# Kernel tuning notes

Measured on AMD Instinct MI355X. Metric: run time of the kernel, lower is better.

Reference implementation:

```python
import jax, jax.numpy as jnp
import numpy as np

MIN_NORM = 1e-15
PROJ_EPS = 4e-3  # hgcn PoincareBall eps for float32
C = 1.0          # curvature (constant across both layers)


def _norm(x):
    return jnp.clip(jnp.linalg.norm(x, axis=-1, keepdims=True), MIN_NORM)


def _artanh(x):
    return jnp.arctanh(jnp.clip(x, -1.0 + 1e-7, 1.0 - 1e-7))


def proj(x, c):
    # clip points inside the Poincare ball of curvature c
    n = _norm(x)
    maxnorm = (1.0 - PROJ_EPS) / jnp.sqrt(c)
    return jnp.where(n > maxnorm, x / n * maxnorm, x)


def expmap0(u, c):
    sc = jnp.sqrt(c)
    n = _norm(u)
    return jnp.tanh(sc * n) * u / (sc * n)


def logmap0(p, c):
    sc = jnp.sqrt(c)
    n = _norm(p)
    return _artanh(sc * n) * p / (sc * n)


def mobius_add(x, y, c):
    x2 = jnp.sum(x * x, -1, keepdims=True)
    y2 = jnp.sum(y * y, -1, keepdims=True)
    xy = jnp.sum(x * y, -1, keepdims=True)
    num = (1.0 + 2.0 * c * xy + c * y2) * x + (1.0 - c * x2) * y
    den = 1.0 + 2.0 * c * xy + (c ** 2) * x2 * y2
    return num / jnp.clip(den, MIN_NORM)


def mobius_matvec(W, x, c):
    sc = jnp.sqrt(c)
    xn = _norm(x)
    mx = x @ W.T
    mxn = _norm(mx)
    res = jnp.tanh(mxn / xn * _artanh(sc * xn)) * mx / (mxn * sc)
    zero = jnp.all(mx == 0, axis=-1, keepdims=True)
    return jnp.where(zero, jnp.zeros((), x.dtype), res)


def hgc_layer(x, W, b, src, dst, ew, c_in, c_out, N):
    # HypLinear: mobius matvec + hyperbolic bias
    h = proj(mobius_matvec(W, x, c_in), c_in)
    hyp_b = proj(expmap0(b[None, :], c_in), c_in)  # proj_tan0 is identity
    h = proj(mobius_add(h, hyp_b, c_in), c_in)
    # HypAgg: tangent-space sparse aggregation
    xt = logmap0(h, c_in)                               # [N, d]
    msg = ew[:, None] * xt[src]                          # [E, d] gather
    agg = jax.ops.segment_sum(msg, dst, num_segments=N)  # spmm(adj, xt)
    h = proj(expmap0(agg, c_in), c_in)
    # HypAct: relu in tangent space, remap with c_out
    xt = jax.nn.relu(logmap0(h, c_in))
    return proj(expmap0(xt, c_out), c_out)


def setup_inputs() -> dict:
    key = jax.random.key(0)
    ks = jax.random.split(key, 8)
    N, F, H, D, E = 100000, 128, 128, 128, 1600000
    s = 1.0 / np.sqrt(F)
    x = jax.random.normal(ks[0], (N, F), jnp.float32) * 0.1
    W1 = jax.random.normal(ks[1], (H, F), jnp.float32) * s
    b1 = jax.random.normal(ks[2], (H,), jnp.float32) * 0.01
    W2 = jax.random.normal(ks[3], (D, H), jnp.float32) * s
    b2 = jax.random.normal(ks[4], (D,), jnp.float32) * 0.01
    edge_weight = jax.random.uniform(ks[5], (E,), jnp.float32) * (1.0 / 16.0)
    src = jax.random.randint(ks[6], (E,), 0, N)
    dst = jax.random.randint(ks[7], (E,), 0, N)
    return {"x": x, "W1": W1, "b1": b1, "W2": W2, "b2": b2,
            "edge_weight": edge_weight, "src": src, "dst": dst}


def reference(x, W1, b1, W2, b2, edge_weight, src, dst):
    N = x.shape[0]
    # HGCN.encode: map Euclidean features onto the manifold
    xh = proj(expmap0(x, C), C)  # proj_tan0 is identity for PoincareBall
    h = hgc_layer(xh, W1, b1, src, dst, edge_weight, C, C, N)
    h = hgc_layer(h, W2, b2, src, dst, edge_weight, C, C, N)
    return h
```

## Files before the change

### kernel.cpp

```cpp
#include <hip/hip_runtime.h>
#include <hip/hip_bf16.h>

#define MINN 1e-15f
#define MAXN (1.0f - 4e-3f)
#define ATMAX 3.1063031f

#define NBH 9
#define BNODES 512
#define BCAP 10240
#define BWIN (BCAP + 4 * BNODES)
#define PBE 8192

typedef short short8 __attribute__((ext_vector_type(8)));
typedef float f32x4 __attribute__((ext_vector_type(4)));

__device__ __forceinline__ float wsum(float v) {
    v += __shfl_xor(v, 32, 64);
    v += __shfl_xor(v, 16, 64);
    v += __shfl_xor(v, 8, 64);
    v += __shfl_xor(v, 4, 64);
    v += __shfl_xor(v, 2, 64);
    v += __shfl_xor(v, 1, 64);
    return v;
}

__device__ __forceinline__ void splitf(float f, short& hi, short& lo) {
    unsigned u = __float_as_uint(f);
    hi = (short)(u >> 16);
    float r = f - __uint_as_float(u & 0xffff0000u);
    lo = (short)(__float_as_uint(r) >> 16);
}

__device__ __forceinline__ unsigned packsplit_hi(short ha, short hb) {
    return (unsigned)(unsigned short)ha | ((unsigned)(unsigned short)hb << 16);
}

__device__ __forceinline__ unsigned pack_bf16(float a, float b) {
    unsigned ua = __float_as_uint(a);
    unsigned ub = __float_as_uint(b);
    ua = (ua + 0x7fffu + ((ua >> 16) & 1u)) >> 16;
    ub = (ub + 0x7fffu + ((ub >> 16) & 1u)) & 0xffff0000u;
    return ua | ub;
}

__device__ __forceinline__ float tanh_fast(float x) {
    float e = __expf(2.f * x);
    return (e - 1.f) * __builtin_amdgcn_rcpf(e + 1.f);
}
__device__ __forceinline__ float atanh_fast(float x) {
    return 0.5f * __logf((1.f + x) * __builtin_amdgcn_rcpf(1.f - x));
}

__global__ __launch_bounds__(256) void k_bucket(const int* __restrict__ src, const int* __restrict__ dst,
                                                const float* __restrict__ ew, int* __restrict__ gcur,
                                                int2* __restrict__ staging, int E, int NBUCK) {
    __shared__ int hist[512];
    const int tid = threadIdx.x;
    const int e0 = blockIdx.x * PBE;
    for (int i = tid; i < 512; i += 256) hist[i] = 0;
    __syncthreads();
    #pragma unroll 4
    for (int j = 0; j < PBE / 256; j++) {
        int e = e0 + j * 256 + tid;
        if (e < E) atomicAdd(&hist[dst[e] >> NBH], 1);
    }
    __syncthreads();
    for (int b = tid; b < NBUCK; b += 256) {
        int c = hist[b];
        hist[b] = c ? atomicAdd(&gcur[b], c) : 0;
    }
    __syncthreads();
    #pragma unroll 4
    for (int j = 0; j < PBE / 256; j++) {
        int e = e0 + j * 256 + tid;
        if (e < E) {
            int d = dst[e];
            int bkt = d >> NBH;
            int pos = atomicAdd(&hist[bkt], 1);
            if (pos < BCAP)
                staging[(size_t)bkt * BCAP + pos] =
                    make_int2((src[e] & 0x1FFFF) | ((d & (BNODES - 1)) << 17), __float_as_int(ew[e]));
        }
    }
}

__global__ __launch_bounds__(256) void k_cbuild(const int* __restrict__ gcur, const int2* __restrict__ staging,
                                                int2* __restrict__ csr, int2* __restrict__ rp2, int N) {
    __shared__ int cnt[BNODES];
    __shared__ int base[BNODES];
    __shared__ int sbuf[256];
    const int tid = threadIdx.x;
    const int b = blockIdx.x;
    const int bcnt = min(gcur[b], BCAP);
    const int wbase = b * BWIN;
    const int2* st = staging + (size_t)b * BCAP;

    for (int i = tid; i < BNODES; i += 256) cnt[i] = 0;
    __syncthreads();
    for (int i = tid; i < bcnt; i += 256) {
        int nl = (st[i].x >> 17) & (BNODES - 1);
        atomicAdd(&cnt[nl], 1);
    }
    __syncthreads();
    int p0 = (cnt[2 * tid] + 3) & ~3;
    int p1 = (cnt[2 * tid + 1] + 3) & ~3;
    int s = p0 + p1;
    sbuf[tid] = s;
    __syncthreads();
    for (int off = 1; off < 256; off <<= 1) {
        int add = (tid >= off) ? sbuf[tid - off] : 0;
        __syncthreads();
        sbuf[tid] += add;
        __syncthreads();
    }
    int excl = sbuf[tid] - s;
    base[2 * tid] = excl;
    base[2 * tid + 1] = excl + p0;
    __syncthreads();
    for (int i = tid; i < BNODES; i += 256) {
        int node = b * BNODES + i;
        int c = cnt[i];
        int pd = (c + 3) & ~3;
        int gb = wbase + base[i];
        if (node < N) rp2[node] = make_int2(gb, pd);
        for (int k = c; k < pd; k++) csr[gb + k] = make_int2(0, 0);
    }
    __syncthreads();
    for (int i = tid; i < BNODES; i += 256) cnt[i] = wbase + base[i];
    __syncthreads();
    for (int i = tid; i < bcnt; i += 256) {
        int2 p = st[i];
        int nl = (p.x >> 17) & (BNODES - 1);
        int pos = atomicAdd(&cnt[nl], 1);
        csr[pos] = make_int2(p.x & 0x1FFFF, p.y);
    }
}

__global__ __launch_bounds__(256) void k_wprep(const float* __restrict__ W1, const float* __restrict__ W2,
                                               unsigned* __restrict__ WH1, unsigned* __restrict__ WL1,
                                               unsigned* __restrict__ WH2, unsigned* __restrict__ WL2) {
    int i = (blockIdx.x & 31) * 256 + threadIdx.x;
    const float* W = (blockIdx.x < 32) ? W1 : W2;
    unsigned* WH = (blockIdx.x < 32) ? WH1 : WH2;
    unsigned* WL = (blockIdx.x < 32) ? WL1 : WL2;
    float a = W[2 * i], b = W[2 * i + 1];
    short ha, la, hb, lb;
    splitf(a, ha, la); splitf(b, hb, lb);
    WH[i] = packsplit_hi(ha, hb);
    WL[i] = packsplit_hi(la, lb);
}

__global__ __launch_bounds__(64) void k_bias(const float* __restrict__ B1, const float* __restrict__ B2,
                                             float2* __restrict__ HB) {
    const int lane = threadIdx.x;
    const float* B = (blockIdx.x == 0) ? B1 : B2;
    float2 bb = *(const float2*)(B + 2 * lane);
    float nb2 = wsum(bb.x * bb.x + bb.y * bb.y);
    float nb = fmaxf(sqrtf(nb2), MINN);
    float tbc = fminf(tanh_fast(nb), MAXN);
    float fb = tbc / nb;
    HB[blockIdx.x * 65 + lane] = make_float2(fb * bb.x, fb * bb.y);
    if (lane == 0) HB[blockIdx.x * 65 + 64] = make_float2(tbc * tbc, 0.f);
}

template <int ENCODE>
__global__ __launch_bounds__(256) void k_linear(
    const float* __restrict__ X,
    const unsigned* __restrict__ XH, const unsigned* __restrict__ XL,
    const unsigned* __restrict__ WH, const unsigned* __restrict__ WL,
    const float2* __restrict__ HB, const float2* __restrict__ NRM,
    unsigned* __restrict__ OUT, int N)
{
    __shared__ float pmn[4][16][4];
    __shared__ float pdm[4][16][4];

    const int lane = threadIdx.x & 63;
    const int wid = threadIdx.x >> 6;
    const int lr = lane & 15;
    const int lg = lane >> 4;
    const int tbase = blockIdx.x * 4;

    short8 Bh[2][4], Bl[2][4];
    #pragma unroll
    for (int ct = 0; ct < 2; ct++) {
        const int nrow = wid * 32 + 2 * lr + ct;
        #pragma unroll
        for (int kt = 0; kt < 4; kt++) {
            Bh[ct][kt] = *(const short8*)(WH + nrow * 64 + kt * 16 + lg * 4);
            Bl[ct][kt] = *(const short8*)(WL + nrow * 64 + kt * 16 + lg * 4);
        }
    }
    const float2 hbc = HB[wid * 16 + lr];
    const float y2 = HB[64].x;

    f32x4 acc[4][2];
    float xnr[4];

    #pragma unroll
    for (int t = 0; t < 4; t++) {
        const int row0 = (tbase + t) << 4;
        if (row0 >= N) break;
        const int arow = min(row0 + lr, N - 1);

        short8 Ah[4], Al[4];
        if (ENCODE) {
            float xn2 = 0.f;
            const float* xr = X + (size_t)arow * 128 + lg * 8;
            #pragma unroll
            for (int kt = 0; kt < 4; kt++) {
                float4 a0 = *(const float4*)(xr + kt * 32);
                float4 a1 = *(const float4*)(xr + kt * 32 + 4);
                float av[8] = {a0.x, a0.y, a0.z, a0.w, a1.x, a1.y, a1.z, a1.w};
                #pragma unroll
                for (int i = 0; i < 8; i++) {
                    xn2 = fmaf(av[i], av[i], xn2);
                    short h, l; splitf(av[i], h, l);
                    Ah[kt][i] = h; Al[kt][i] = l;
                }
            }
            xn2 += __shfl_xor(xn2, 16, 64);
            xn2 += __shfl_xor(xn2, 32, 64);
            xnr[t] = xn2;
        } else {
            #pragma unroll
            for (int kt = 0; kt < 4; kt++) {
                Ah[kt] = *(const short8*)(XH + (size_t)arow * 64 + kt * 16 + lg * 4);
                Al[kt] = *(const short8*)(XL + (size_t)arow * 64 + kt * 16 + lg * 4);
            }
        }

        f32x4 a0 = {0.f, 0.f, 0.f, 0.f}, a1 = {0.f, 0.f, 0.f, 0.f};
        #pragma unroll
        for (int kt = 0; kt < 4; kt++) {
            a0 = __builtin_amdgcn_mfma_f32_16x16x32_bf16(Ah[kt], Bh[0][kt], a0, 0, 0, 0);
            a1 = __builtin_amdgcn_mfma_f32_16x16x32_bf16(Ah[kt], Bh[1][kt], a1, 0, 0, 0);
            a0 = __builtin_amdgcn_mfma_f32_16x16x32_bf16(Al[kt], Bh[0][kt], a0, 0, 0, 0);
            a1 = __builtin_amdgcn_mfma_f32_16x16x32_bf16(Al[kt], Bh[1][kt], a1, 0, 0, 0);
            a0 = __builtin_amdgcn_mfma_f32_16x16x32_bf16(Ah[kt], Bl[0][kt], a0, 0, 0, 0);
            a1 = __builtin_amdgcn_mfma_f32_16x16x32_bf16(Ah[kt], Bl[1][kt], a1, 0, 0, 0);
        }
        acc[t][0] = a0; acc[t][1] = a1;

        float pm[4], pd[4];
        #pragma unroll
        for (int r = 0; r < 4; r++) {
            pm[r] = a0[r] * a0[r] + a1[r] * a1[r];
            pd[r] = a0[r] * hbc.x + a1[r] * hbc.y;
        }
        #pragma unroll
        for (int s = 1; s <= 8; s <<= 1) {
            #pragma unroll
            for (int r = 0; r < 4; r++) {
                pm[r] += __shfl_xor(pm[r], s, 64);
                pd[r] += __shfl_xor(pd[r], s, 64);
            }
        }
        if (lr == 0) {
            #pragma unroll
            for (int r = 0; r < 4; r++) {
                pmn[t][lg * 4 + r][wid] = pm[r];
                pdm[t][lg * 4 + r][wid] = pd[r];
            }
        }
    }
    __syncthreads();

    #pragma unroll
    for (int t = 0; t < 4; t++) {
        const int row0 = (tbase + t) << 4;
        if (row0 >= N) break;

        float4 qm = *(const float4*)pmn[t][lr];
        float4 qd = *(const float4*)pdm[t][lr];
        float mn2 = (qm.x + qm.y) + (qm.z + qm.w);
        float dmb = (qd.x + qd.y) + (qd.z + qd.w);
        const int crow = row0 + lr;
        float caf1 = 0.f, cbs = 0.f;
        if (crow < N) {
            float xn, axn;
            if (ENCODE) {
                float n0 = fmaxf(sqrtf(xnr[t]), MINN);
                xn = n0;
                axn = fminf(n0, ATMAX);
            } else {
                float2 nr = NRM[crow];
                xn = fmaxf(nr.x, MINN);
                axn = nr.y;
            }
            float mxn = fmaxf(sqrtf(mn2), MINN);
            float arg = (mxn / xn) * axn;
            float thc = fminf(tanh_fast(arg), MAXN);
            float f1 = thc / mxn;
            float x2 = thc * thc;
            float xy = f1 * dmb;
            float ca = 1.f + 2.f * xy + y2;
            float cb = 1.f - x2;
            float inv = 1.f / fmaxf(1.f + 2.f * xy + x2 * y2, MINN);
            float ng2 = inv * inv * (ca * ca * x2 + 2.f * ca * cb * xy + cb * cb * y2);
            float ng = fmaxf(sqrtf(ng2), MINN);
            float lf = atanh_fast(fminf(ng, MAXN)) / ng;
            float sle = lf * inv;
            caf1 = sle * ca * f1;
            cbs = sle * cb;
        }
        #pragma unroll
        for (int r = 0; r < 4; r++) {
            const int q = lg * 4 + r;
            float c1 = __shfl(caf1, q, 16);
            float c2 = __shfl(cbs, q, 16);
            const int row = row0 + q;
            if (row < N) {
                float o0 = c1 * acc[t][0][r] + c2 * hbc.x;
                float o1 = c1 * acc[t][1][r] + c2 * hbc.y;
                OUT[(size_t)row * 64 + wid * 16 + lr] = pack_bf16(o0, o1);
            }
        }
    }
}

__global__ __launch_bounds__(256) void k_aggact(const unsigned* __restrict__ XT, const int2* __restrict__ rp2,
                                                const int2* __restrict__ csr,
                                                float* __restrict__ OUTF,
                                                unsigned* __restrict__ OUTH, unsigned* __restrict__ OUTL,
                                                float2* __restrict__ NRM, int N, int last) {
    const int lane = threadIdx.x & 63;
    const int wid = threadIdx.x >> 6;
    int node = blockIdx.x * 4 + wid;
    if (node >= N) return;
    int2 rr = rp2[node];
    int b = __builtin_amdgcn_readfirstlane(rr.x);
    int cnt = __builtin_amdgcn_readfirstlane(rr.y);
    int e8 = b + (cnt & ~7);

    float ax[8], ay[8];
    #pragma unroll
    for (int j = 0; j < 8; j++) { ax[j] = 0.f; ay[j] = 0.f; }

    for (int i = b; i < e8; i += 8) {
        int2 c[8];
        #pragma unroll
        for (int j = 0; j < 8; j++) c[j] = csr[i + j];
        unsigned v[8];
        #pragma unroll
        for (int j = 0; j < 8; j++) v[j] = XT[(size_t)c[j].x * 64 + lane];
        #pragma unroll
        for (int j = 0; j < 8; j++) {
            float w = __int_as_float(c[j].y);
            ax[j] = fmaf(w, __uint_as_float(v[j] << 16), ax[j]);
            ay[j] = fmaf(w, __uint_as_float(v[j] & 0xffff0000u), ay[j]);
        }
    }
    if (cnt & 4) {
        int i = e8;
        int2 c[4];
        #pragma unroll
        for (int j = 0; j < 4; j++) c[j] = csr[i + j];
        unsigned v[4];
        #pragma unroll
        for (int j = 0; j < 4; j++) v[j] = XT[(size_t)c[j].x * 64 + lane];
        #pragma unroll
        for (int j = 0; j < 4; j++) {
            float w = __int_as_float(c[j].y);
            ax[j] = fmaf(w, __uint_as_float(v[j] << 16), ax[j]);
            ay[j] = fmaf(w, __uint_as_float(v[j] & 0xffff0000u), ay[j]);
        }
    }
    float a0 = ((ax[0] + ax[1]) + (ax[2] + ax[3])) + ((ax[4] + ax[5]) + (ax[6] + ax[7]));
    float a1 = ((ay[0] + ay[1]) + (ay[2] + ay[3])) + ((ay[4] + ay[5]) + (ay[6] + ay[7]));

    float r0 = fmaxf(a0, 0.f), r1 = fmaxf(a1, 0.f);
    float n2 = a0 * a0 + a1 * a1;
    float q2 = r0 * r0 + r1 * r1;
    #pragma unroll
    for (int s = 32; s; s >>= 1) {
        n2 += __shfl_xor(n2, s, 64);
        q2 += __shfl_xor(q2, s, 64);
    }
    float n = fmaxf(sqrtf(n2), MINN);
    float cp = fminf(n, ATMAX) / n;
    float nq = fmaxf(cp * sqrtf(q2), MINN);
    float tq = fminf(tanh_fast(nq), MAXN);
    float f2 = tq / nq;
    float sc = f2 * cp;
    float o0 = sc * r0, o1 = sc * r1;
    if (last) {
        *(float2*)(OUTF + (size_t)node * 128 + 2 * lane) = make_float2(o0, o1);
    } else {
        short h0, l0, h1, l1;
        splitf(o0, h0, l0); splitf(o1, h1, l1);
        OUTH[(size_t)node * 64 + lane] = packsplit_hi(h0, h1);
        OUTL[(size_t)node * 64 + lane] = packsplit_hi(l0, l1);
        if (lane == 0) NRM[node] = make_float2(tq, fminf(nq, ATMAX));
    }
}

extern "C" void kernel_launch(void* const* d_in, const int* in_sizes, int n_in,
                              void* d_out, int out_size, void* d_ws, size_t ws_size,
                              hipStream_t stream) {
    const float* x  = (const float*)d_in[0];
    const float* W1 = (const float*)d_in[1];
    const float* b1 = (const float*)d_in[2];
    const float* W2 = (const float*)d_in[3];
    const float* b2 = (const float*)d_in[4];
    const float* ew = (const float*)d_in[5];
    const int* src  = (const int*)d_in[6];
    const int* dst  = (const int*)d_in[7];
    const int N = in_sizes[0] / 128;
    const int E = in_sizes[5];
    float* out = (float*)d_out;

    const int NBUCK = (N + BNODES - 1) >> NBH;
    const int EB = (E + PBE - 1) / PBE;

    char* w = (char*)d_ws;
    unsigned* xt  = (unsigned*)w; w += (size_t)N * 64 * 4;
    unsigned* xh  = (unsigned*)w; w += (size_t)N * 64 * 4;
    unsigned* xl  = (unsigned*)w; w += (size_t)N * 64 * 4;
    int2*   csr   = (int2*)w;   w += (size_t)NBUCK * BWIN * 8;
    float2* nrm   = (float2*)w; w += (size_t)N * 8;
    int2*   rp2   = (int2*)w;   w += (size_t)N * 8;
    int2*   staging = (int2*)w; w += (size_t)NBUCK * BCAP * 8;
    unsigned* wh1 = (unsigned*)w; w += 8192 * 4;
    unsigned* wl1 = (unsigned*)w; w += 8192 * 4;
    unsigned* wh2 = (unsigned*)w; w += 8192 * 4;
    unsigned* wl2 = (unsigned*)w; w += 8192 * 4;
    float2* hbuf  = (float2*)w; w += 2 * 65 * 8;
    int*    gcur  = (int*)w;    w += (size_t)NBUCK * 4 + 256;

    hipMemsetAsync(gcur, 0, (size_t)NBUCK * 4, stream);
    k_bucket<<<EB, 256, 0, stream>>>(src, dst, ew, gcur, staging, E, NBUCK);
    k_cbuild<<<NBUCK, 256, 0, stream>>>(gcur, staging, csr, rp2, N);
    k_wprep<<<64, 256, 0, stream>>>(W1, W2, wh1, wl1, wh2, wl2);
    k_bias<<<2, 64, 0, stream>>>(b1, b2, hbuf);

    const int rowblocks = (N + 3) / 4;
    const int ntiles = (N + 15) / 16;
    const int nlb = (ntiles + 3) / 4;

    k_linear<1><<<nlb, 256, 0, stream>>>(x, nullptr, nullptr, wh1, wl1, hbuf, nullptr, xt, N);
    k_aggact<<<rowblocks, 256, 0, stream>>>(xt, rp2, csr, nullptr, xh, xl, nrm, N, 0);
    k_linear<0><<<nlb, 256, 0, stream>>>(nullptr, xh, xl, wh2, wl2, hbuf + 65, nrm, xt, N);
    k_aggact<<<rowblocks, 256, 0, stream>>>(xt, rp2, csr, out, nullptr, nullptr, nullptr, N, 1);
}
```

Before: 300.9 us.

## Store split-bf16 activations and weights in MFMA fragment order; add separate encode pass

Activations (hi/lo bf16 split) and weight matrices are now written in a fragment-major layout, so each lane's MFMA operand load becomes a contiguous 16-byte read at fragment base plus lane*4. Encoding of the input x moves out of the first linear kernel into a new k_encode kernel that splits values and records norms, so one k_linear serves both layers. The aim is coalesced operand loads in k_linear. The cost is an extra launch plus writing and rereading the split input, and aggact now does scattered fragment-index stores.

```diff
diff --git a/kernel.cpp b/kernel.cpp
--- a/kernel.cpp
+++ b/kernel.cpp
@@ -49,6 +49,10 @@
 }
 __device__ __forceinline__ float atanh_fast(float x) {
     return 0.5f * __logf((1.f + x) * __builtin_amdgcn_rcpf(1.f - x));
+}
+
+__device__ __forceinline__ size_t fragidx(int row, int c) {
+    return ((size_t)((row >> 4) * 4 + (c >> 4)) << 8) + ((((c >> 2) & 3) * 16 + (row & 15)) << 2) + (c & 3);
 }
 
 __global__ __launch_bounds__(256) void k_bucket(const int* __restrict__ src, const int* __restrict__ dst,
@@ -139,15 +143,21 @@
 __global__ __launch_bounds__(256) void k_wprep(const float* __restrict__ W1, const float* __restrict__ W2,
                                                unsigned* __restrict__ WH1, unsigned* __restrict__ WL1,
                                                unsigned* __restrict__ WH2, unsigned* __restrict__ WL2) {
-    int i = (blockIdx.x & 31) * 256 + threadIdx.x;
+    int f = (blockIdx.x & 31) * 256 + threadIdx.x;
     const float* W = (blockIdx.x < 32) ? W1 : W2;
     unsigned* WH = (blockIdx.x < 32) ? WH1 : WH2;
     unsigned* WL = (blockIdx.x < 32) ? WL1 : WL2;
-    float a = W[2 * i], b = W[2 * i + 1];
+    int frag = f >> 8, rem = f & 255;
+    int lane = rem >> 2, j = rem & 3;
+    int lr = lane & 15, lg = lane >> 4;
+    int wid = frag >> 3, ct = (frag >> 2) & 1, kt = frag & 3;
+    int n = wid * 32 + 2 * lr + ct;
+    int c = kt * 16 + lg * 4 + j;
+    float a = W[n * 128 + 2 * c], b = W[n * 128 + 2 * c + 1];
     short ha, la, hb, lb;
     splitf(a, ha, la); splitf(b, hb, lb);
-    WH[i] = packsplit_hi(ha, hb);
-    WL[i] = packsplit_hi(la, lb);
+    WH[f] = packsplit_hi(ha, hb);
+    WL[f] = packsplit_hi(la, lb);
 }
 
 __global__ __launch_bounds__(64) void k_bias(const float* __restrict__ B1, const float* __restrict__ B2,
@@ -163,11 +173,29 @@
     if (lane == 0) HB[blockIdx.x * 65 + 64] = make_float2(tbc * tbc, 0.f);
 }
 
-template <int ENCODE>
+__global__ __launch_bounds__(256) void k_encode(const float* __restrict__ X,
+                                                unsigned* __restrict__ XH, unsigned* __restrict__ XL,
+                                                float2* __restrict__ NRM, int N) {
+    const int lane = threadIdx.x & 63;
+    const int wid = threadIdx.x >> 6;
+    int row = blockIdx.x * 4 + wid;
+    if (row >= N) return;
+    float2 u = *(const float2*)(X + (size_t)row * 128 + 2 * lane);
+    float n2 = wsum(u.x * u.x + u.y * u.y);
+    short h0, l0, h1, l1;
+    splitf(u.x, h0, l0); splitf(u.y, h1, l1);
+    size_t idx = fragidx(row, lane);
+    XH[idx] = packsplit_hi(h0, h1);
+    XL[idx] = packsplit_hi(l0, l1);
+    if (lane == 0) {
+        float n0 = fmaxf(sqrtf(n2), MINN);
+        NRM[row] = make_float2(n0, fminf(n0, ATMAX));
+    }
+}
+
 __global__ __launch_bounds__(256) void k_linear(
-    const float* __restrict__ X,
-    const unsigned* __restrict__ XH, const unsigned* __restrict__ XL,
-    const unsigned* __restrict__ WH, const unsigned* __restrict__ WL,
+    const unsigned* __restrict__ XHf, const unsigned* __restrict__ XLf,
+    const unsigned* __restrict__ WHf, const unsigned* __restrict__ WLf,
     const float2* __restrict__ HB, const float2* __restrict__ NRM,
     unsigned* __restrict__ OUT, int N)
 {
@@ -183,50 +211,29 @@
     short8 Bh[2][4], Bl[2][4];
     #pragma unroll
     for (int ct = 0; ct < 2; ct++) {
-        const int nrow = wid * 32 + 2 * lr + ct;
         #pragma unroll
         for (int kt = 0; kt < 4; kt++) {
-            Bh[ct][kt] = *(const short8*)(WH + nrow * 64 + kt * 16 + lg * 4);
-            Bl[ct][kt] = *(const short8*)(WL + nrow * 64 + kt * 16 + lg * 4);
+            const int fb = ((wid * 2 + ct) * 4 + kt) << 8;
+            Bh[ct][kt] = *(const short8*)(WHf + fb + lane * 4);
+            Bl[ct][kt] = *(const short8*)(WLf + fb + lane * 4);
         }
     }
     const float2 hbc = HB[wid * 16 + lr];
     const float y2 = HB[64].x;
 
     f32x4 acc[4][2];
-    float xnr[4];
 
     #pragma unroll
     for (int t = 0; t < 4; t++) {
         const int row0 = (tbase + t) << 4;
         if (row0 >= N) break;
-        const int arow = min(row0 + lr, N - 1);
 
         short8 Ah[4], Al[4];
-        if (ENCODE) {
-            float xn2 = 0.f;
-            const float* xr = X + (size_t)arow * 128 + lg * 8;
-            #pragma unroll
-            for (int kt = 0; kt < 4; kt++) {
-                float4 a0 = *(const float4*)(xr + kt * 32);
-                float4 a1 = *(const float4*)(xr + kt * 32 + 4);
-                float av[8] = {a0.x, a0.y, a0.z, a0.w, a1.x, a1.y, a1.z, a1.w};
-                #pragma unroll
-                for (int i = 0; i < 8; i++) {
-                    xn2 = fmaf(av[i], av[i], xn2);
-                    short h, l; splitf(av[i], h, l);
-                    Ah[kt][i] = h; Al[kt][i] = l;
-                }
-            }
-            xn2 += __shfl_xor(xn2, 16, 64);
-            xn2 += __shfl_xor(xn2, 32, 64);
-            xnr[t] = xn2;
-        } else {
-            #pragma unroll
-            for (int kt = 0; kt < 4; kt++) {
-                Ah[kt] = *(const short8*)(XH + (size_t)arow * 64 + kt * 16 + lg * 4);
-                Al[kt] = *(const short8*)(XL + (size_t)arow * 64 + kt * 16 + lg * 4);
-            }
+        #pragma unroll
+        for (int kt = 0; kt < 4; kt++) {
+            const int fa = ((tbase + t) * 4 + kt) << 8;
+            Ah[kt] = *(const short8*)(XHf + fa + lane * 4);
+            Al[kt] = *(const short8*)(XLf + fa + lane * 4);
         }
 
         f32x4 a0 = {0.f, 0.f, 0.f, 0.f}, a1 = {0.f, 0.f, 0.f, 0.f};
@@ -277,16 +284,9 @@
         const int crow = row0 + lr;
         float caf1 = 0.f, cbs = 0.f;
         if (crow < N) {
-            float xn, axn;
-            if (ENCODE) {
-                float n0 = fmaxf(sqrtf(xnr[t]), MINN);
-                xn = n0;
-                axn = fminf(n0, ATMAX);
-            } else {
-                float2 nr = NRM[crow];
-                xn = fmaxf(nr.x, MINN);
-                axn = nr.y;
-            }
+            float2 nr = NRM[crow];
+            float xn = fmaxf(nr.x, MINN);
+            float axn = nr.y;
             float mxn = fmaxf(sqrtf(mn2), MINN);
             float arg = (mxn / xn) * axn;
             float thc = fminf(tanh_fast(arg), MAXN);
@@ -388,8 +388,9 @@
     } else {
         short h0, l0, h1, l1;
         splitf(o0, h0, l0); splitf(o1, h1, l1);
-        OUTH[(size_t)node * 64 + lane] = packsplit_hi(h0, h1);
-        OUTL[(size_t)node * 64 + lane] = packsplit_hi(l0, l1);
+        size_t idx = fragidx(node, lane);
+        OUTH[idx] = packsplit_hi(h0, h1);
+        OUTL[idx] = packsplit_hi(l0, l1);
         if (lane == 0) NRM[node] = make_float2(tq, fminf(nq, ATMAX));
     }
 }
@@ -411,11 +412,12 @@
 
     const int NBUCK = (N + BNODES - 1) >> NBH;
     const int EB = (E + PBE - 1) / PBE;
+    const int ntiles = (N + 15) / 16;
 
     char* w = (char*)d_ws;
     unsigned* xt  = (unsigned*)w; w += (size_t)N * 64 * 4;
-    unsigned* xh  = (unsigned*)w; w += (size_t)N * 64 * 4;
-    unsigned* xl  = (unsigned*)w; w += (size_t)N * 64 * 4;
+    unsigned* xhf = (unsigned*)w; w += (size_t)ntiles * 1024 * 4;
+    unsigned* xlf = (unsigned*)w; w += (size_t)ntiles * 1024 * 4;
     int2*   csr   = (int2*)w;   w += (size_t)NBUCK * BWIN * 8;
     float2* nrm   = (float2*)w; w += (size_t)N * 8;
     int2*   rp2   = (int2*)w;   w += (size_t)N * 8;
@@ -434,11 +436,11 @@
     k_bias<<<2, 64, 0, stream>>>(b1, b2, hbuf);
 
     const int rowblocks = (N + 3) / 4;
-    const int ntiles = (N + 15) / 16;
     const int nlb = (ntiles + 3) / 4;
 
-    k_linear<1><<<nlb, 256, 0, stream>>>(x, nullptr, nullptr, wh1, wl1, hbuf, nullptr, xt, N);
-    k_aggact<<<rowblocks, 256, 0, stream>>>(xt, rp2, csr, nullptr, xh, xl, nrm, N, 0);
-    k_linear<0><<<nlb, 256, 0, stream>>>(nullptr, xh, xl, wh2, wl2, hbuf + 65, nrm, xt, N);
+    k_encode<<<rowblocks, 256, 0, stream>>>(x, xhf, xlf, nrm, N);
+    k_linear<<<nlb, 256, 0, stream>>>(xhf, xlf, wh1, wl1, hbuf, nrm, xt, N);
+    k_aggact<<<rowblocks, 256, 0, stream>>>(xt, rp2, csr, nullptr, xhf, xlf, nrm, N, 0);
+    k_linear<<<nlb, 256, 0, stream>>>(xhf, xlf, wh2, wl2, hbuf + 65, nrm, xt, N);
     k_aggact<<<rowblocks, 256, 0, stream>>>(xt, rp2, csr, out, nullptr, nullptr, nullptr, N, 1);
 }
```

Measured after the change: 286.4 us. 4.8% less time.
